# Kernel tuning notes

Hardware: AMD Instinct MI355X
Metric: run time of the kernel (lower is better)

Reference implementation:

```python
import jax, jax.numpy as jnp
import numpy as np

B, C, H, L = 4, 1, 1024, 8192
KD, NS = 64, 4  # kernel_dim, num_scales


def _interp_linear(x, out_len):
    """F.interpolate(mode='linear', align_corners=False) along last axis."""
    in_len = x.shape[-1]
    if out_len == in_len:
        return x
    scale = out_len / in_len
    coord = (jnp.arange(out_len, dtype=jnp.float32) + 0.5) / scale - 0.5
    coord = jnp.clip(coord, 0.0, in_len - 1)
    lo = jnp.floor(coord).astype(jnp.int32)
    hi = jnp.minimum(lo + 1, in_len - 1)
    w = coord - lo.astype(jnp.float32)
    return x[..., lo] * (1.0 - w) + x[..., hi] * w


def setup_inputs() -> dict:
    key = jax.random.key(0)
    ks = jax.random.split(key, 8)
    u = jax.random.normal(ks[0], (B, H, L), jnp.float32)
    k0 = jax.random.normal(ks[1], (C, H, KD), jnp.float32)
    k1 = jax.random.normal(ks[2], (C, H, KD), jnp.float32)
    k2 = jax.random.normal(ks[3], (C, H, KD), jnp.float32)
    k3 = jax.random.normal(ks[4], (C, H, KD), jnp.float32)
    D = jax.random.normal(ks[5], (C, H), jnp.float32)
    W = jax.random.normal(ks[6], (H, C * H), jnp.float32) / np.float32(np.sqrt(C * H))
    b = jnp.zeros((H,), jnp.float32)
    return {"u": u, "k0": k0, "k1": k1, "k2": k2, "k3": k3, "D": D, "W": W, "b": b}


def reference(u, k0, k1, k2, k3, D, W, b):
    Lq = u.shape[-1]
    kernels = [k0, k1, k2, k3]
    total = KD * 2 ** (NS - 1)  # 512
    # multi-scale kernel build: interpolate -> right-pad -> scale -> sum
    parts = []
    for i in range(NS):
        ki = _interp_linear(kernels[i], KD * 2 ** i)
        ki = jnp.pad(ki, ((0, 0), (0, 0), (0, total - KD * 2 ** i)))
        parts.append(ki * (2.0 ** (NS - i - 1)))
    k = parts[0] + parts[1] + parts[2] + parts[3]  # (C,H,512)
    # fit to sequence length L
    if k.shape[-1] > Lq:
        k = k[..., :Lq]
    elif k.shape[-1] < Lq:
        k = jnp.pad(k, ((0, 0), (0, 0), (0, Lq - k.shape[-1])))
    # detached kernel norm
    knorm = jax.lax.stop_gradient(
        jnp.linalg.norm(k, axis=-1, keepdims=True))
    k = k / knorm
    # FFT long convolution
    n = 2 * Lq
    k_f = jnp.fft.rfft(k, n=n)              # (C,H,L+1) complex
    u_f = jnp.fft.rfft(u, n=n)              # (B,H,L+1) complex
    y_f = jnp.einsum('bhl,chl->bchl', u_f, k_f)
    y = jnp.fft.irfft(y_f, n=n)[..., :Lq]   # (B,C,H,L)
    # D skip (outer product)
    y = y + jnp.einsum('bhl,ch->bchl', u, D)
    y = y.reshape(y.shape[0], C * H, Lq)    # (B,C*H,L)
    # activation (exact gelu, torch default), dropout=Identity, norm=Identity
    y = jax.nn.gelu(y, approximate=False)
    # output_linear: 1x1 conv (C*H -> H) with bias, Identity post-activation
    y = jnp.einsum('bfl,of->bol', y, W) + b[None, :, None]
    return y
```

## Files before the change

### kernel.cpp

```cpp
#include <hip/hip_runtime.h>
#include <cstdint>
#include <cstddef>

#define HH 1024
#define LL 8192
#define NB 4
#define KD 64
#define KLEN 512
#define LHALF 4096

typedef float v4f  __attribute__((ext_vector_type(4)));
typedef float v16f __attribute__((ext_vector_type(16)));
typedef short v8s  __attribute__((ext_vector_type(8)));

__device__ __forceinline__ unsigned short f2bf(float f) {
  union { float f; unsigned int u; } x; x.f = f;
  unsigned int r = x.u + 0x7fffu + ((x.u >> 16) & 1u);
  return (unsigned short)(r >> 16);
}

__device__ __forceinline__ float bfbits2f(unsigned int hi16) {
  union { unsigned int u; float f; } x; x.u = hi16;
  return x.f;
}

__device__ __forceinline__ float gelu_f(float y) {
  float x = y * 0.70710678118654752f;
  float ax = fabsf(x);
  float t = __builtin_amdgcn_rcpf(fmaf(0.3275911f, ax, 1.0f));
  float p = t * fmaf(t, fmaf(t, fmaf(t, fmaf(t, 1.061405429f, -1.453152027f),
                                     1.421413741f), -0.284496736f), 0.254829592f);
  float e = __expf(-x * x);
  float erfax = fmaf(-p, e, 1.0f);
  float er = copysignf(erfax, x);
  return 0.5f * y * (1.0f + er);
}

__global__ void w2bf_kernel(const float* __restrict__ W,
                            unsigned short* __restrict__ Wb, int n) {
  int i = blockIdx.x * blockDim.x + threadIdx.x;
  if (i < n) Wb[i] = f2bf(W[i]);
}

__device__ __forceinline__ int suswz(int b) { return b ^ (((b >> 7) & 3) << 4); }

__global__ __launch_bounds__(256) void conv_kernel(
    const float* __restrict__ k0, const float* __restrict__ k1,
    const float* __restrict__ k2, const float* __restrict__ k3,
    const float* __restrict__ u, const float* __restrict__ D,
    unsigned short* __restrict__ g) {
  __shared__ __align__(16) unsigned short Apk[34 * 512];
  __shared__ __align__(16) unsigned short su[512 + LHALF];
  __shared__ __align__(16) float skk[KLEN];
  __shared__ float lk[4][KD];
  __shared__ float sred[4];

  const int bid = blockIdx.x;
  const int h = bid >> 1;
  const int half = bid & 1;
  const int l0 = half * LHALF;
  const int tid = threadIdx.x;
  const int w = tid >> 6;
  const int ln = tid & 63;
  const int n = ln & 31;
  const int q = ln >> 5;
  char* sub = (char*)su;

  {
    int i = tid >> 6, j = tid & 63;
    const float* src = (i == 0) ? k0 : (i == 1) ? k1 : (i == 2) ? k2 : k3;
    lk[i][j] = src[h * KD + j];
  }
  __syncthreads();
  float ss = 0.f;
  for (int tt = tid; tt < KLEN; tt += 256) {
    float kt = 0.f;
#pragma unroll
    for (int i = 0; i < 4; i++) {
      int len = KD << i;
      if (tt < len) {
        float inv = 1.0f / (float)(1 << i);
        float c = ((float)tt + 0.5f) * inv - 0.5f;
        c = fminf(fmaxf(c, 0.0f), 63.0f);
        int lo = (int)floorf(c);
        int hi = min(lo + 1, 63);
        float wq = c - (float)lo;
        kt += (lk[i][lo] * (1.0f - wq) + lk[i][hi] * wq) * (float)(1 << (3 - i));
      }
    }
    skk[tt] = kt;
    ss += kt * kt;
  }
#pragma unroll
  for (int off = 32; off > 0; off >>= 1) ss += __shfl_xor(ss, off);
  if (ln == 0) sred[w] = ss;
  __syncthreads();
  const float invn = 1.0f / sqrtf(sred[0] + sred[1] + sred[2] + sred[3]);

#pragma unroll 4
  for (int e = 0; e < 68; ++e) {
    int idx = e * 256 + tid;
    int s = idx >> 9;
    int lane = (idx >> 3) & 63;
    int j = idx & 7;
    int m = lane & 31, q2 = lane >> 5;
    int c = ((s & 1) << 4) + (q2 << 3) + j;
    int t = ((s >> 1) << 5) + m - c;
    Apk[idx] = (t >= 0 && t < KLEN) ? f2bf(skk[t] * invn) : (unsigned short)0;
  }

  const float Dh = D[h];
  const int bbyte0 = 1024 + 64 * (w * 32 + n) + 16 * q;

  for (int b = 0; b < NB; ++b) {
    __syncthreads();
    const float* __restrict__ urow = u + ((size_t)b * HH + h) * LL;
    if (tid < 128) {
      int i = tid * 4;
      uint2 p;
      if (half == 0) {
        p.x = 0u; p.y = 0u;
      } else {
        float4 v = *(const float4*)(urow + l0 - 512 + i);
        p.x = (unsigned)f2bf(v.x) | ((unsigned)f2bf(v.y) << 16);
        p.y = (unsigned)f2bf(v.z) | ((unsigned)f2bf(v.w) << 16);
      }
      *(uint2*)(sub + suswz(2 * i)) = p;
    }
#pragma unroll
    for (int r = 0; r < 4; ++r) {
      int i = r * 1024 + tid * 4;
      float4 v = *(const float4*)(urow + l0 + i);
      uint2 p;
      p.x = (unsigned)f2bf(v.x) | ((unsigned)f2bf(v.y) << 16);
      p.y = (unsigned)f2bf(v.z) | ((unsigned)f2bf(v.w) << 16);
      *(uint2*)(sub + suswz(1024 + 2 * i)) = p;
    }
    __syncthreads();

    v16f acc;
#pragma unroll
    for (int r = 0; r < 16; ++r) acc[r] = 0.f;

#pragma unroll
    for (int s = 0; s < 34; ++s) {
      const int offb = ((s & 1) << 5) - ((s >> 1) << 6);
      v8s af = *(const v8s*)(Apk + (s << 9) + (ln << 3));
      v8s b0 = *(const v8s*)(sub + suswz(bbyte0 + offb));
      acc = __builtin_amdgcn_mfma_f32_32x32x16_bf16(af, b0, acc, 0, 0, 0);
    }

    unsigned short* grow = g + ((size_t)b * HH + h) * LL + l0;
#pragma unroll
    for (int rg = 0; rg < 4; ++rg) {
      const int l = 32 * (w * 32 + n) + 8 * rg + 4 * q;
      uint2 up2 = *(const uint2*)(sub + suswz(1024 + 2 * l));
      float uf[4];
      uf[0] = bfbits2f(up2.x << 16);
      uf[1] = bfbits2f(up2.x & 0xffff0000u);
      uf[2] = bfbits2f(up2.y << 16);
      uf[3] = bfbits2f(up2.y & 0xffff0000u);
      unsigned short hb[4];
#pragma unroll
      for (int rr = 0; rr < 4; ++rr) {
        float y = acc[rg * 4 + rr] + Dh * uf[rr];
        hb[rr] = f2bf(gelu_f(y));
      }
      uint2 p;
      p.x = (unsigned)hb[0] | ((unsigned)hb[1] << 16);
      p.y = (unsigned)hb[2] | ((unsigned)hb[3] << 16);
      *(uint2*)(grow + l) = p;
    }
  }
}

__device__ __forceinline__ void gll16(const void* g, void* l) {
  __builtin_amdgcn_global_load_lds(
      (const __attribute__((address_space(1))) unsigned int*)g,
      (__attribute__((address_space(3))) unsigned int*)l, 16, 0, 0);
}

__global__ __launch_bounds__(256, 4) void gemm_kernel(
    const unsigned short* __restrict__ A,
    const unsigned short* __restrict__ G,
    const float* __restrict__ bias, float* __restrict__ out) {
  __shared__ __align__(16) unsigned short sA[2][4096];
  __shared__ __align__(16) unsigned int   sB[2][1024];
  const int tid = threadIdx.x;
  const int wv = tid >> 6, ln = tid & 63;

  const int bid0 = blockIdx.x;
  const int swz = (bid0 & 7) * 512 + (bid0 >> 3);
  const int mt = swz & 7, nt = swz >> 3;
  const int o0 = mt * 128;
  const int bb = nt >> 7;
  const int l0 = (nt & 127) * 64;
  const int m16 = ln & 15, q4 = ln >> 4;
  const int wm = wv & 1, wn = wv >> 1;

  v4f acc[4][2];
#pragma unroll
  for (int i = 0; i < 4; i++)
#pragma unroll
    for (int j = 0; j < 2; j++) {
      v4f z = {0.f, 0.f, 0.f, 0.f};
      acc[i][j] = z;
    }

  const unsigned short* gA[2];
  int lA[2];
  {
    const int cc = (((ln & 3) ^ ((ln >> 3) & 3)) << 3);
#pragma unroll
    for (int qq = 0; qq < 2; qq++) {
      const int c = wv * 2 + qq;
      const int rr = c * 16 + (ln >> 2);
      gA[qq] = A + (size_t)(o0 + rr) * HH + cc;
      lA[qq] = c * 512;
    }
  }

  const int pr = tid >> 3;
  const int seg = tid & 7;
  const unsigned short* gB0 = G + ((size_t)bb * HH + 2 * pr) * LL + l0 + seg * 8;
  const unsigned short* gB1 = gB0 + LL;

  int aby[4], bby[2];
#pragma unroll
  for (int i = 0; i < 4; i++) {
    int row = wm * 64 + i * 16 + m16;
    aby[i] = (row * 64 + q4 * 16) ^ (((m16 >> 1) & 3) << 4);
  }
#pragma unroll
  for (int j = 0; j < 2; j++) {
    int l = wn * 32 + j * 16 + m16;
    bby[j] = (l * 64 + q4 * 16) ^ (((l >> 3) & 3) << 5);
  }

  auto stageA = [&](int buf, int kbase) {
#pragma unroll
    for (int qq = 0; qq < 2; qq++) gll16(gA[qq] + kbase, &sA[buf][lA[qq]]);
  };
  auto packB = [&](int buf, const uint4& r0, const uint4& r1) {
    union { uint4 u; unsigned short s[8]; } ua, ub; ua.u = r0; ub.u = r1;
    char* base = (char*)sB[buf];
#pragma unroll
    for (int e = 0; e < 8; e++) {
      int l = seg * 8 + e;
      unsigned v = (unsigned)ua.s[e] | ((unsigned)ub.s[e] << 16);
      *(unsigned*)(base + ((l * 64 + pr * 4) ^ ((seg & 3) << 5))) = v;
    }
  };

  uint4 c0, c1;
  stageA(0, 0);
  __builtin_amdgcn_sched_barrier(0);
  if (wv < 2) {
    uint4 p0 = *(const uint4*)(gB0);
    uint4 p1 = *(const uint4*)(gB1);
    c0 = *(const uint4*)(gB0 + (size_t)32 * LL);
    c1 = *(const uint4*)(gB1 + (size_t)32 * LL);
    packB(0, p0, p1);
    asm volatile("s_waitcnt vmcnt(2)" ::: "memory");
  } else {
    asm volatile("s_waitcnt vmcnt(0)" ::: "memory");
  }
  asm volatile("s_waitcnt lgkmcnt(0)" ::: "memory");
  __builtin_amdgcn_s_barrier();

  for (int kk = 0; kk < 30; ++kk) {
    const int p = kk & 1;
    v8s af[4], bf[2];
    const char* ab = (const char*)sA[p];
    const char* bbc = (const char*)sB[p];
#pragma unroll
    for (int i = 0; i < 4; i++) af[i] = *(const v8s*)(ab + aby[i]);
#pragma unroll
    for (int j = 0; j < 2; j++) bf[j] = *(const v8s*)(bbc + bby[j]);
    stageA(p ^ 1, (kk + 1) * 32);
    __builtin_amdgcn_sched_barrier(0);
    uint4 n0, n1;
    if (wv < 2) {
      n0 = *(const uint4*)(gB0 + (size_t)(kk + 2) * 32 * LL);
      n1 = *(const uint4*)(gB1 + (size_t)(kk + 2) * 32 * LL);
    }
    asm volatile("s_waitcnt lgkmcnt(0)" ::: "memory");
    __builtin_amdgcn_sched_barrier(0);
    __builtin_amdgcn_s_setprio(1);
#pragma unroll
    for (int i = 0; i < 4; i++)
#pragma unroll
      for (int j = 0; j < 2; j++)
        acc[i][j] = __builtin_amdgcn_mfma_f32_16x16x32_bf16(af[i], bf[j], acc[i][j], 0, 0, 0);
    __builtin_amdgcn_s_setprio(0);
    if (wv < 2) {
      asm volatile("s_waitcnt vmcnt(4)" ::: "memory");
      packB(p ^ 1, c0, c1);
      c0 = n0; c1 = n1;
      asm volatile("s_waitcnt vmcnt(2) lgkmcnt(0)" ::: "memory");
    } else {
      asm volatile("s_waitcnt vmcnt(0) lgkmcnt(0)" ::: "memory");
    }
    __builtin_amdgcn_s_barrier();
  }

  {
    v8s af[4], bf[2];
    const char* ab = (const char*)sA[0];
    const char* bbc = (const char*)sB[0];
#pragma unroll
    for (int i = 0; i < 4; i++) af[i] = *(const v8s*)(ab + aby[i]);
#pragma unroll
    for (int j = 0; j < 2; j++) bf[j] = *(const v8s*)(bbc + bby[j]);
    stageA(1, 31 * 32);
    asm volatile("s_waitcnt lgkmcnt(0)" ::: "memory");
    __builtin_amdgcn_sched_barrier(0);
    __builtin_amdgcn_s_setprio(1);
#pragma unroll
    for (int i = 0; i < 4; i++)
#pragma unroll
      for (int j = 0; j < 2; j++)
        acc[i][j] = __builtin_amdgcn_mfma_f32_16x16x32_bf16(af[i], bf[j], acc[i][j], 0, 0, 0);
    __builtin_amdgcn_s_setprio(0);
    if (wv < 2) {
      asm volatile("s_waitcnt vmcnt(2)" ::: "memory");
      packB(1, c0, c1);
    }
    asm volatile("s_waitcnt vmcnt(0) lgkmcnt(0)" ::: "memory");
    __builtin_amdgcn_s_barrier();
  }
  {
    v8s af[4], bf[2];
    const char* ab = (const char*)sA[1];
    const char* bbc = (const char*)sB[1];
#pragma unroll
    for (int i = 0; i < 4; i++) af[i] = *(const v8s*)(ab + aby[i]);
#pragma unroll
    for (int j = 0; j < 2; j++) bf[j] = *(const v8s*)(bbc + bby[j]);
    asm volatile("s_waitcnt lgkmcnt(0)" ::: "memory");
    __builtin_amdgcn_sched_barrier(0);
    __builtin_amdgcn_s_setprio(1);
#pragma unroll
    for (int i = 0; i < 4; i++)
#pragma unroll
      for (int j = 0; j < 2; j++)
        acc[i][j] = __builtin_amdgcn_mfma_f32_16x16x32_bf16(af[i], bf[j], acc[i][j], 0, 0, 0);
    __builtin_amdgcn_s_setprio(0);
  }

#pragma unroll
  for (int i = 0; i < 4; i++) {
    const int ob = o0 + wm * 64 + i * 16 + q4 * 4;
#pragma unroll
    for (int j = 0; j < 2; j++) {
      const int l = l0 + wn * 32 + j * 16 + m16;
#pragma unroll
      for (int r = 0; r < 4; r++) {
        const int o = ob + r;
        out[((size_t)bb * HH + o) * LL + l] = acc[i][j][r] + bias[o];
      }
    }
  }
}

extern "C" void kernel_launch(void* const* d_in, const int* in_sizes, int n_in,
                              void* d_out, int out_size, void* d_ws, size_t ws_size,
                              hipStream_t stream) {
  const float* u   = (const float*)d_in[0];
  const float* k0  = (const float*)d_in[1];
  const float* k1  = (const float*)d_in[2];
  const float* k2  = (const float*)d_in[3];
  const float* k3  = (const float*)d_in[4];
  const float* D   = (const float*)d_in[5];
  const float* W   = (const float*)d_in[6];
  const float* bia = (const float*)d_in[7];
  float* out = (float*)d_out;

  char* ws = (char*)d_ws;
  unsigned short* g  = (unsigned short*)ws;
  unsigned short* Wb = (unsigned short*)(ws + (size_t)67108864);

  w2bf_kernel<<<(HH * HH + 255) / 256, 256, 0, stream>>>(W, Wb, HH * HH);
  conv_kernel<<<HH * 2, 256, 0, stream>>>(k0, k1, k2, k3, u, D, g);
  gemm_kernel<<<8 * 512, 256, 0, stream>>>(Wb, g, bia, out);
}
```

Before: 390.0 us.

## Enlarge GEMM tile to 128x128 with BK=64 and all-wave B staging

The GEMM block tile grows from 128x64 to 128x128 and the K step from 32 to 64, halving the grid and the loop trip count. Each wave now runs 32 MFMAs per step, and all four waves load and transpose-pack the B operand with a new XOR swizzle. The goal is more operand reuse per byte loaded and fewer barriers per FLOP. In exchange, LDS use roughly quadruples and register pressure rises (the launch-bounds occupancy hint is removed), which lowers occupancy.

```diff
diff --git a/kernel.cpp b/kernel.cpp
--- a/kernel.cpp
+++ b/kernel.cpp
@@ -180,171 +180,195 @@
       (__attribute__((address_space(3))) unsigned int*)l, 16, 0, 0);
 }
 
-__global__ __launch_bounds__(256, 4) void gemm_kernel(
+__global__ __launch_bounds__(256) void gemm_kernel(
     const unsigned short* __restrict__ A,
     const unsigned short* __restrict__ G,
     const float* __restrict__ bias, float* __restrict__ out) {
-  __shared__ __align__(16) unsigned short sA[2][4096];
-  __shared__ __align__(16) unsigned int   sB[2][1024];
+  __shared__ __align__(16) unsigned short sA[2][8192];
+  __shared__ __align__(16) unsigned int   sB[2][4096];
   const int tid = threadIdx.x;
   const int wv = tid >> 6, ln = tid & 63;
 
   const int bid0 = blockIdx.x;
-  const int swz = (bid0 & 7) * 512 + (bid0 >> 3);
+  const int swz = (bid0 & 7) * 256 + (bid0 >> 3);
   const int mt = swz & 7, nt = swz >> 3;
   const int o0 = mt * 128;
-  const int bb = nt >> 7;
-  const int l0 = (nt & 127) * 64;
+  const int bb = nt >> 6;
+  const int l0 = (nt & 63) * 128;
   const int m16 = ln & 15, q4 = ln >> 4;
   const int wm = wv & 1, wn = wv >> 1;
 
-  v4f acc[4][2];
+  v4f acc[4][4];
 #pragma unroll
   for (int i = 0; i < 4; i++)
 #pragma unroll
-    for (int j = 0; j < 2; j++) {
+    for (int j = 0; j < 4; j++) {
       v4f z = {0.f, 0.f, 0.f, 0.f};
       acc[i][j] = z;
     }
 
-  const unsigned short* gA[2];
-  int lA[2];
+  const unsigned short* gA[4];
+  int lA[4];
   {
-    const int cc = (((ln & 3) ^ ((ln >> 3) & 3)) << 3);
-#pragma unroll
-    for (int qq = 0; qq < 2; qq++) {
-      const int c = wv * 2 + qq;
-      const int rr = c * 16 + (ln >> 2);
+    const int cc = (((ln & 7) ^ (ln >> 3)) << 3);
+#pragma unroll
+    for (int qq = 0; qq < 4; qq++) {
+      const int c = wv * 4 + qq;
+      const int rr = c * 8 + (ln >> 3);
       gA[qq] = A + (size_t)(o0 + rr) * HH + cc;
       lA[qq] = c * 512;
     }
   }
 
-  const int pr = tid >> 3;
-  const int seg = tid & 7;
-  const unsigned short* gB0 = G + ((size_t)bb * HH + 2 * pr) * LL + l0 + seg * 8;
-  const unsigned short* gB1 = gB0 + LL;
-
-  int aby[4], bby[2];
+  const int hq = tid & 15;
+  const int seg = tid >> 4;
+  const unsigned short* gB[4];
+#pragma unroll
+  for (int jj = 0; jj < 4; jj++)
+    gB[jj] = G + ((size_t)bb * HH + 4 * hq + jj) * LL + l0 + seg * 8;
+
+  int aby[4], bby[4];
 #pragma unroll
   for (int i = 0; i < 4; i++) {
     int row = wm * 64 + i * 16 + m16;
-    aby[i] = (row * 64 + q4 * 16) ^ (((m16 >> 1) & 3) << 4);
-  }
-#pragma unroll
-  for (int j = 0; j < 2; j++) {
-    int l = wn * 32 + j * 16 + m16;
-    bby[j] = (l * 64 + q4 * 16) ^ (((l >> 3) & 3) << 5);
+    aby[i] = (row * 128 + q4 * 16) ^ ((row & 7) << 4);
+  }
+#pragma unroll
+  for (int j = 0; j < 4; j++) {
+    int l = wn * 64 + j * 16 + m16;
+    bby[j] = (l * 128 + q4 * 16) ^ ((l & 7) << 4);
   }
 
   auto stageA = [&](int buf, int kbase) {
 #pragma unroll
-    for (int qq = 0; qq < 2; qq++) gll16(gA[qq] + kbase, &sA[buf][lA[qq]]);
+    for (int qq = 0; qq < 4; qq++) gll16(gA[qq] + kbase, &sA[buf][lA[qq]]);
   };
-  auto packB = [&](int buf, const uint4& r0, const uint4& r1) {
-    union { uint4 u; unsigned short s[8]; } ua, ub; ua.u = r0; ub.u = r1;
+  auto packB = [&](int buf, const uint4& r0, const uint4& r1,
+                   const uint4& r2, const uint4& r3) {
+    union { uint4 u; unsigned short s[8]; } u0, u1, u2, u3;
+    u0.u = r0; u1.u = r1; u2.u = r2; u3.u = r3;
     char* base = (char*)sB[buf];
 #pragma unroll
     for (int e = 0; e < 8; e++) {
       int l = seg * 8 + e;
-      unsigned v = (unsigned)ua.s[e] | ((unsigned)ub.s[e] << 16);
-      *(unsigned*)(base + ((l * 64 + pr * 4) ^ ((seg & 3) << 5))) = v;
+      uint2 v;
+      v.x = (unsigned)u0.s[e] | ((unsigned)u1.s[e] << 16);
+      v.y = (unsigned)u2.s[e] | ((unsigned)u3.s[e] << 16);
+      *(uint2*)(base + ((l * 128 + hq * 8) ^ ((e & 7) << 4))) = v;
     }
   };
 
-  uint4 c0, c1;
+  uint4 c0, c1, c2, c3;
   stageA(0, 0);
   __builtin_amdgcn_sched_barrier(0);
-  if (wv < 2) {
-    uint4 p0 = *(const uint4*)(gB0);
-    uint4 p1 = *(const uint4*)(gB1);
-    c0 = *(const uint4*)(gB0 + (size_t)32 * LL);
-    c1 = *(const uint4*)(gB1 + (size_t)32 * LL);
-    packB(0, p0, p1);
-    asm volatile("s_waitcnt vmcnt(2)" ::: "memory");
-  } else {
-    asm volatile("s_waitcnt vmcnt(0)" ::: "memory");
-  }
+  uint4 p0 = *(const uint4*)(gB[0]);
+  uint4 p1 = *(const uint4*)(gB[1]);
+  uint4 p2 = *(const uint4*)(gB[2]);
+  uint4 p3 = *(const uint4*)(gB[3]);
+  c0 = *(const uint4*)(gB[0] + (size_t)64 * LL);
+  c1 = *(const uint4*)(gB[1] + (size_t)64 * LL);
+  c2 = *(const uint4*)(gB[2] + (size_t)64 * LL);
+  c3 = *(const uint4*)(gB[3] + (size_t)64 * LL);
+  __builtin_amdgcn_sched_barrier(0);
+  asm volatile("s_waitcnt vmcnt(4)" ::: "memory");
+  packB(0, p0, p1, p2, p3);
   asm volatile("s_waitcnt lgkmcnt(0)" ::: "memory");
   __builtin_amdgcn_s_barrier();
 
-  for (int kk = 0; kk < 30; ++kk) {
+  for (int kk = 0; kk < 14; ++kk) {
     const int p = kk & 1;
-    v8s af[4], bf[2];
+    v8s af[4][2], bf[4][2];
     const char* ab = (const char*)sA[p];
     const char* bbc = (const char*)sB[p];
 #pragma unroll
-    for (int i = 0; i < 4; i++) af[i] = *(const v8s*)(ab + aby[i]);
-#pragma unroll
-    for (int j = 0; j < 2; j++) bf[j] = *(const v8s*)(bbc + bby[j]);
-    stageA(p ^ 1, (kk + 1) * 32);
+    for (int i = 0; i < 4; i++) {
+      af[i][0] = *(const v8s*)(ab + aby[i]);
+      af[i][1] = *(const v8s*)(ab + (aby[i] ^ 64));
+    }
+#pragma unroll
+    for (int j = 0; j < 4; j++) {
+      bf[j][0] = *(const v8s*)(bbc + bby[j]);
+      bf[j][1] = *(const v8s*)(bbc + (bby[j] ^ 64));
+    }
+    stageA(p ^ 1, (kk + 1) * 64);
     __builtin_amdgcn_sched_barrier(0);
-    uint4 n0, n1;
-    if (wv < 2) {
-      n0 = *(const uint4*)(gB0 + (size_t)(kk + 2) * 32 * LL);
-      n1 = *(const uint4*)(gB1 + (size_t)(kk + 2) * 32 * LL);
-    }
+    uint4 n0 = *(const uint4*)(gB[0] + (size_t)(kk + 2) * 64 * LL);
+    uint4 n1 = *(const uint4*)(gB[1] + (size_t)(kk + 2) * 64 * LL);
+    uint4 n2 = *(const uint4*)(gB[2] + (size_t)(kk + 2) * 64 * LL);
+    uint4 n3 = *(const uint4*)(gB[3] + (size_t)(kk + 2) * 64 * LL);
     asm volatile("s_waitcnt lgkmcnt(0)" ::: "memory");
     __builtin_amdgcn_sched_barrier(0);
     __builtin_amdgcn_s_setprio(1);
 #pragma unroll
-    for (int i = 0; i < 4; i++)
-#pragma unroll
-      for (int j = 0; j < 2; j++)
-        acc[i][j] = __builtin_amdgcn_mfma_f32_16x16x32_bf16(af[i], bf[j], acc[i][j], 0, 0, 0);
+    for (int kh = 0; kh < 2; kh++)
+#pragma unroll
+      for (int i = 0; i < 4; i++)
+#pragma unroll
+        for (int j = 0; j < 4; j++)
+          acc[i][j] = __builtin_amdgcn_mfma_f32_16x16x32_bf16(af[i][kh], bf[j][kh], acc[i][j], 0, 0, 0);
     __builtin_amdgcn_s_setprio(0);
-    if (wv < 2) {
-      asm volatile("s_waitcnt vmcnt(4)" ::: "memory");
-      packB(p ^ 1, c0, c1);
-      c0 = n0; c1 = n1;
-      asm volatile("s_waitcnt vmcnt(2) lgkmcnt(0)" ::: "memory");
-    } else {
-      asm volatile("s_waitcnt vmcnt(0) lgkmcnt(0)" ::: "memory");
-    }
+    asm volatile("s_waitcnt vmcnt(8)" ::: "memory");
+    packB(p ^ 1, c0, c1, c2, c3);
+    c0 = n0; c1 = n1; c2 = n2; c3 = n3;
+    asm volatile("s_waitcnt vmcnt(4) lgkmcnt(0)" ::: "memory");
     __builtin_amdgcn_s_barrier();
   }
 
   {
-    v8s af[4], bf[2];
+    v8s af[4][2], bf[4][2];
     const char* ab = (const char*)sA[0];
     const char* bbc = (const char*)sB[0];
 #pragma unroll
-    for (int i = 0; i < 4; i++) af[i] = *(const v8s*)(ab + aby[i]);
-#pragma unroll
-    for (int j = 0; j < 2; j++) bf[j] = *(const v8s*)(bbc + bby[j]);
-    stageA(1, 31 * 32);
+    for (int i = 0; i < 4; i++) {
+      af[i][0] = *(const v8s*)(ab + aby[i]);
+      af[i][1] = *(const v8s*)(ab + (aby[i] ^ 64));
+    }
+#pragma unroll
+    for (int j = 0; j < 4; j++) {
+      bf[j][0] = *(const v8s*)(bbc + bby[j]);
+      bf[j][1] = *(const v8s*)(bbc + (bby[j] ^ 64));
+    }
+    stageA(1, 15 * 64);
     asm volatile("s_waitcnt lgkmcnt(0)" ::: "memory");
     __builtin_amdgcn_sched_barrier(0);
     __builtin_amdgcn_s_setprio(1);
 #pragma unroll
-    for (int i = 0; i < 4; i++)
-#pragma unroll
-      for (int j = 0; j < 2; j++)
-        acc[i][j] = __builtin_amdgcn_mfma_f32_16x16x32_bf16(af[i], bf[j], acc[i][j], 0, 0, 0);
+    for (int kh = 0; kh < 2; kh++)
+#pragma unroll
+      for (int i = 0; i < 4; i++)
+#pragma unroll
+        for (int j = 0; j < 4; j++)
+          acc[i][j] = __builtin_amdgcn_mfma_f32_16x16x32_bf16(af[i][kh], bf[j][kh], acc[i][j], 0, 0, 0);
     __builtin_amdgcn_s_setprio(0);
-    if (wv < 2) {
-      asm volatile("s_waitcnt vmcnt(2)" ::: "memory");
-      packB(1, c0, c1);
-    }
+    asm volatile("s_waitcnt vmcnt(4)" ::: "memory");
+    packB(1, c0, c1, c2, c3);
     asm volatile("s_waitcnt vmcnt(0) lgkmcnt(0)" ::: "memory");
     __builtin_amdgcn_s_barrier();
   }
   {
-    v8s af[4], bf[2];
+    v8s af[4][2], bf[4][2];
     const char* ab = (const char*)sA[1];
     const char* bbc = (const char*)sB[1];
 #pragma unroll
-    for (int i = 0; i < 4; i++) af[i] = *(const v8s*)(ab + aby[i]);
-#pragma unroll
-    for (int j = 0; j < 2; j++) bf[j] = *(const v8s*)(bbc + bby[j]);
+    for (int i = 0; i < 4; i++) {
+      af[i][0] = *(const v8s*)(ab + aby[i]);
+      af[i][1] = *(const v8s*)(ab + (aby[i] ^ 64));
+    }
+#pragma unroll
+    for (int j = 0; j < 4; j++) {
+      bf[j][0] = *(const v8s*)(bbc + bby[j]);
+      bf[j][1] = *(const v8s*)(bbc + (bby[j] ^ 64));
+    }
     asm volatile("s_waitcnt lgkmcnt(0)" ::: "memory");
     __builtin_amdgcn_sched_barrier(0);
     __builtin_amdgcn_s_setprio(1);
 #pragma unroll
-    for (int i = 0; i < 4; i++)
-#pragma unroll
-      for (int j = 0; j < 2; j++)
-        acc[i][j] = __builtin_amdgcn_mfma_f32_16x16x32_bf16(af[i], bf[j], acc[i][j], 0, 0, 0);
+    for (int kh = 0; kh < 2; kh++)
+#pragma unroll
+      for (int i = 0; i < 4; i++)
+#pragma unroll
+        for (int j = 0; j < 4; j++)
+          acc[i][j] = __builtin_amdgcn_mfma_f32_16x16x32_bf16(af[i][kh], bf[j][kh], acc[i][j], 0, 0, 0);
     __builtin_amdgcn_s_setprio(0);
   }
 
@@ -352,8 +376,8 @@
   for (int i = 0; i < 4; i++) {
     const int ob = o0 + wm * 64 + i * 16 + q4 * 4;
 #pragma unroll
-    for (int j = 0; j < 2; j++) {
-      const int l = l0 + wn * 32 + j * 16 + m16;
+    for (int j = 0; j < 4; j++) {
+      const int l = l0 + wn * 64 + j * 16 + m16;
 #pragma unroll
       for (int r = 0; r < 4; r++) {
         const int o = ob + r;
@@ -382,5 +406,5 @@
 
   w2bf_kernel<<<(HH * HH + 255) / 256, 256, 0, stream>>>(W, Wb, HH * HH);
   conv_kernel<<<HH * 2, 256, 0, stream>>>(k0, k1, k2, k3, u, D, g);
-  gemm_kernel<<<8 * 512, 256, 0, stream>>>(Wb, g, bia, out);
-}
+  gemm_kernel<<<8 * 256, 256, 0, stream>>>(Wb, g, bia, out);
+}
```

Measured after the change: 425.2 us. 1.09x slower.
